# Kernel optimization log

Measured on AMD Instinct MI355X. Metric: run time of the kernel, lower is better.

Reference implementation:

```python
import jax, jax.numpy as jnp
import numpy as np

B, C, D, H, W = 4, 128, 16, 16, 16
HID = 128
EPS = 1e-5


def setup_inputs() -> dict:
    key = jax.random.key(0)
    ks = jax.random.split(key, 10)
    s = 1.0 / np.sqrt(C)
    return {
        "x": jax.random.normal(ks[0], (B, C, D, H, W), dtype=jnp.float32),
        "Wq": jax.random.normal(ks[1], (HID, C), dtype=jnp.float32) * s,
        "bq": jax.random.normal(ks[2], (HID,), dtype=jnp.float32) * s,
        "Wk": jax.random.normal(ks[3], (HID, C), dtype=jnp.float32) * s,
        "bk": jax.random.normal(ks[4], (HID,), dtype=jnp.float32) * s,
        "Wv": jax.random.normal(ks[5], (HID, C), dtype=jnp.float32) * s,
        "bv": jax.random.normal(ks[6], (HID,), dtype=jnp.float32) * s,
        "bn_weight": jax.random.normal(ks[7], (HID,), dtype=jnp.float32),
        "bn_bias": jax.random.normal(ks[8], (HID,), dtype=jnp.float32),
        "gamma": jax.random.normal(ks[9], (1,), dtype=jnp.float32),
    }


def reference(x, Wq, bq, Wk, bk, Wv, bv, bn_weight, bn_bias, gamma):
    b, c, d, h, w = x.shape
    n = d * h * w
    xf = x.reshape(b, c, n)  # [B, C, N]
    # 1x1 conv3d == per-voxel linear: [B, hid, N]
    q = jnp.einsum("hc,bcn->bnh", Wq, xf) + bq  # [B, N, hid] (query permuted)
    k = jnp.einsum("hc,bcn->bhn", Wk, xf) + bk[None, :, None]  # [B, hid, N]
    v = jnp.einsum("hc,bcn->bhn", Wv, xf) + bv[None, :, None]  # [B, hid, N]
    # unscaled attention scores [B, N, N], softmax over last dim
    attn = jax.nn.softmax(jnp.einsum("bih,bhj->bij", q, k), axis=-1)
    # out[b,h,i] = sum_j v[b,h,j] * attn[b,i,j]
    out = jnp.einsum("bhj,bij->bhi", v, attn)  # [B, hid, N]
    # BatchNorm3d (training mode): per-channel stats over (B, N), biased var
    mean = jnp.mean(out, axis=(0, 2), keepdims=True)
    var = jnp.mean(jnp.square(out - mean), axis=(0, 2), keepdims=True)
    out = (out - mean) * jax.lax.rsqrt(var + EPS)
    out = out * bn_weight[None, :, None] + bn_bias[None, :, None]
    out = gamma[0] * out.reshape(b, c, d, h, w) + x
    return out
```

## Files before the change

kernel.cpp:

```cpp
#include <hip/hip_runtime.h>


#define NV 4096
#define LOG2E 1.44269504088896340736f
#define EPSV 1e-5f

typedef float f32x4 __attribute__((ext_vector_type(4)));
typedef short bf16x8 __attribute__((ext_vector_type(8)));
typedef unsigned short u16x4 __attribute__((ext_vector_type(4)));

static __device__ __forceinline__ unsigned short f2bf(float f) {
    union { float f; unsigned u; } v; v.f = f;
    unsigned r = v.u + 0x7FFFu + ((v.u >> 16) & 1u);
    return (unsigned short)(r >> 16);
}
static __device__ __forceinline__ float bf2f(unsigned short u) {
    union { unsigned u; float f; } v; v.u = ((unsigned)u) << 16; return v.f;
}

__global__ __launch_bounds__(256) void convw_kernel(
    const float* __restrict__ Wq, const float* __restrict__ Wk,
    const float* __restrict__ Wv, unsigned short* __restrict__ Wbf)
{
    int i = blockIdx.x * 256 + threadIdx.x;
    const float* src = (i < 16384) ? Wq : (i < 32768 ? Wk : Wv);
    Wbf[i] = f2bf(src[i & 16383]);
}

__global__ __launch_bounds__(256) void xt_kernel(
    const float* __restrict__ x, unsigned short* __restrict__ xT)
{
    __shared__ unsigned short st[64 * 132];
    const int b = blockIdx.x >> 6, n0 = (blockIdx.x & 63) << 6;
    const int t = threadIdx.x;
    #pragma unroll
    for (int it = 0; it < 32; ++it) {
        const int e = it * 256 + t;
        const int c = e >> 6, il = e & 63;
        st[il * 132 + c] = f2bf(x[(((b << 7) + c) << 12) + n0 + il]);
    }
    __syncthreads();
    unsigned short* dst = xT + (((b << 12) + n0) << 7);
    #pragma unroll
    for (int it = 0; it < 32; ++it) {
        const int e = it * 256 + t;
        const int il = e >> 7, c = e & 127;
        dst[(il << 7) + c] = st[il * 132 + c];
    }
}

__global__ __launch_bounds__(256) void proj_kernel(
    const unsigned short* __restrict__ xT,
    const unsigned short* __restrict__ Wbf,
    const float* __restrict__ bq, const float* __restrict__ bk,
    const float* __restrict__ bv,
    unsigned short* __restrict__ Qb, unsigned short* __restrict__ Kb,
    unsigned short* __restrict__ Vb)
{
    __shared__ unsigned short vtile[128 * 66];
    const int bid = blockIdx.x;
    const int m = bid >> 8, b = (bid >> 6) & 3, n0 = (bid & 63) << 6;
    const int t = threadIdx.x, w = t >> 6, lane = t & 63;
    const int quad = lane >> 4, l16 = lane & 15;
    const int vb = n0 + (w << 4);

    bf16x8 af[4];
    {
        const unsigned short* xr = xT + (((b << 12) + vb + l16) << 7) + (quad << 3);
        #pragma unroll
        for (int ck = 0; ck < 4; ++ck) af[ck] = *(const bf16x8*)(xr + (ck << 5));
    }
    const unsigned short* Wm = Wbf + (m << 14);
    const float* bias = (m == 0) ? bq : ((m == 1) ? bk : bv);
    unsigned short* dst = (m == 0) ? Qb : Kb;

    #pragma unroll
    for (int s = 0; s < 8; ++s) {
        const int h = (s << 4) + l16;
        f32x4 acc = {0.f, 0.f, 0.f, 0.f};
        #pragma unroll
        for (int ck = 0; ck < 4; ++ck) {
            bf16x8 wf = *(const bf16x8*)(Wm + (h << 7) + (ck << 5) + (quad << 3));
            acc = __builtin_amdgcn_mfma_f32_16x16x32_bf16(af[ck], wf, acc, 0, 0, 0);
        }
        const float bval = bias[h];
        if (m == 2) {
            #pragma unroll
            for (int r = 0; r < 4; ++r)
                vtile[h * 66 + (w << 4) + (quad << 2) + r] = f2bf(acc[r] + bval);
        } else {
            #pragma unroll
            for (int r = 0; r < 4; ++r) {
                const int n = vb + (quad << 2) + r;
                dst[(((b << 12) + n) << 7) + h] = f2bf(acc[r] + bval);
            }
        }
    }
    if (m == 2) {
        __syncthreads();
        #pragma unroll
        for (int it = 0; it < 32; ++it) {
            const int e = it * 256 + t;
            const int h = e >> 6, il = e & 63;
            Vb[(((b << 7) + h) << 12) + n0 + il] = vtile[h * 66 + il];
        }
    }
}

template<int NSL>
__global__ __launch_bounds__(256, 2) void flash_kernel(
    const unsigned short* __restrict__ Qb,
    const unsigned short* __restrict__ Kb,
    const unsigned short* __restrict__ Vb,
    float* __restrict__ Opart, float* __restrict__ lpart,
    unsigned short* __restrict__ Obuf)
{
    __shared__ unsigned short Kt[64 * 128];
    __shared__ unsigned short Vt[128 * 64];
    __shared__ unsigned short pA[4][32 * 72];
    const int bid = blockIdx.x;
    const int sl = bid >> 7, b = (bid >> 5) & 3, ic = bid & 31;
    const int t = threadIdx.x, w = t >> 6, lane = t & 63;
    const int quad = lane >> 4, l16 = lane & 15;
    const int iw = (ic << 7) + (w << 5);
    const int jbase = sl * (NV / NSL);
    unsigned short* pAw = pA[w];

    const int ktg = t & 15, ktj = t >> 4;
    const int vtg = t & 7,  vth = t >> 3;
    const int kswz = (ktg ^ ktj) << 3;
    const int vswz = (vtg ^ (vth & 7)) << 3;

    bf16x8 qf[2][4];
    #pragma unroll
    for (int half = 0; half < 2; ++half) {
        const unsigned short* qp =
            Qb + (((b << 12) + iw + (half << 4) + l16) << 7) + (quad << 3);
        #pragma unroll
        for (int ck = 0; ck < 4; ++ck) qf[half][ck] = *(const bf16x8*)(qp + (ck << 5));
    }
    f32x4 Oacc[2][8];
    #pragma unroll
    for (int half = 0; half < 2; ++half)
        #pragma unroll
        for (int s = 0; s < 8; ++s) Oacc[half][s] = (f32x4){0.f, 0.f, 0.f, 0.f};
    float lsum0 = 0.f, lsum1 = 0.f;

    const unsigned short* Kbb = Kb + ((long)b << 19);
    const unsigned short* Vbb = Vb + ((long)b << 19);

    for (int t8 = 0; t8 < (NV / NSL) >> 6; ++t8) {
        const int j0 = jbase + (t8 << 6);

        __syncthreads();
        bf16x8 sk[4], sv[4];
        #pragma unroll
        for (int r = 0; r < 4; ++r)
            sk[r] = *(const bf16x8*)(Kbb + ((j0 + (r << 4) + ktj) << 7) + (ktg << 3));
        #pragma unroll
        for (int r = 0; r < 4; ++r)
            sv[r] = *(const bf16x8*)(Vbb + (((r << 5) + vth) << 12) + j0 + (vtg << 3));
        #pragma unroll
        for (int r = 0; r < 4; ++r)
            *(bf16x8*)(Kt + (((r << 4) + ktj) << 7) + kswz) = sk[r];
        #pragma unroll
        for (int r = 0; r < 4; ++r)
            *(bf16x8*)(Vt + (((r << 5) + vth) << 6) + vswz) = sv[r];
        __syncthreads();

        #pragma unroll
        for (int js = 0; js < 4; ++js) {
            bf16x8 kf[4];
            const int krow = ((js << 4) + l16) << 7;
            #pragma unroll
            for (int ck = 0; ck < 4; ++ck)
                kf[ck] = *(const bf16x8*)(Kt + krow + ((((ck << 2) + quad) ^ l16) << 3));
            f32x4 a0 = {0.f, 0.f, 0.f, 0.f}, a1 = {0.f, 0.f, 0.f, 0.f};
            #pragma unroll
            for (int ck = 0; ck < 4; ++ck) {
                a0 = __builtin_amdgcn_mfma_f32_16x16x32_bf16(kf[ck], qf[0][ck], a0, 0, 0, 0);
                a1 = __builtin_amdgcn_mfma_f32_16x16x32_bf16(kf[ck], qf[1][ck], a1, 0, 0, 0);
            }
            u16x4 pk0, pk1;
            float ls0 = 0.f, ls1 = 0.f;
            #pragma unroll
            for (int r = 0; r < 4; ++r) {
                const unsigned short u0 = f2bf(exp2f(a0[r] * LOG2E));
                const unsigned short u1 = f2bf(exp2f(a1[r] * LOG2E));
                pk0[r] = u0; ls0 += bf2f(u0);
                pk1[r] = u1; ls1 += bf2f(u1);
            }
            lsum0 += ls0; lsum1 += ls1;
            const int jc = (js << 4) + (quad << 2);
            *(u16x4*)(pAw + l16 * 72 + jc)        = pk0;
            *(u16x4*)(pAw + (16 + l16) * 72 + jc) = pk1;
        }
        bf16x8 pf[2][2];
        #pragma unroll
        for (int half = 0; half < 2; ++half)
            #pragma unroll
            for (int kh = 0; kh < 2; ++kh)
                pf[half][kh] = *(const bf16x8*)(pAw + ((half << 4) + l16) * 72 +
                                                (kh << 5) + (quad << 3));
        #pragma unroll
        for (int s = 0; s < 8; ++s) {
            const int vrow = ((s << 4) + l16) << 6;
            const bf16x8 v0 = *(const bf16x8*)(Vt + vrow + ((quad ^ (l16 & 7)) << 3));
            const bf16x8 v1 = *(const bf16x8*)(Vt + vrow + (((4 + quad) ^ (l16 & 7)) << 3));
            Oacc[0][s] = __builtin_amdgcn_mfma_f32_16x16x32_bf16(v0, pf[0][0], Oacc[0][s], 0, 0, 0);
            Oacc[0][s] = __builtin_amdgcn_mfma_f32_16x16x32_bf16(v1, pf[0][1], Oacc[0][s], 0, 0, 0);
            Oacc[1][s] = __builtin_amdgcn_mfma_f32_16x16x32_bf16(v0, pf[1][0], Oacc[1][s], 0, 0, 0);
            Oacc[1][s] = __builtin_amdgcn_mfma_f32_16x16x32_bf16(v1, pf[1][1], Oacc[1][s], 0, 0, 0);
        }
    }

    float l0 = lsum0; l0 += __shfl_xor(l0, 16); l0 += __shfl_xor(l0, 32);
    float l1 = lsum1; l1 += __shfl_xor(l1, 16); l1 += __shfl_xor(l1, 32);

    if (NSL == 1) {
        const float rl0 = 1.f / l0, rl1 = 1.f / l1;
        #pragma unroll
        for (int s = 0; s < 8; ++s)
            #pragma unroll
            for (int r = 0; r < 4; ++r) {
                const int h = (s << 4) + (quad << 2) + r;
                Obuf[(((b << 7) + h) << 12) + iw + l16]      = f2bf(Oacc[0][s][r] * rl0);
                Obuf[(((b << 7) + h) << 12) + iw + 16 + l16] = f2bf(Oacc[1][s][r] * rl1);
            }
    } else {
        const int slb = (sl << 2) + b;
        if (quad == 0) {
            lpart[(slb << 12) + iw + l16]      = l0;
            lpart[(slb << 12) + iw + 16 + l16] = l1;
        }
        float* Ob = Opart + ((long)slb << 19);
        #pragma unroll
        for (int half = 0; half < 2; ++half)
            #pragma unroll
            for (int s = 0; s < 8; ++s)
                #pragma unroll
                for (int r = 0; r < 4; ++r) {
                    const int h = (s << 4) + (quad << 2) + r;
                    Ob[(h << 12) + iw + (half << 4) + l16] = Oacc[half][s][r];
                }
    }
}

template<int NSL>
__global__ __launch_bounds__(256) void merge_kernel(
    const float* __restrict__ Opart, const float* __restrict__ lpart,
    unsigned short* __restrict__ Obuf, float* __restrict__ psums)
{
    const int bid = blockIdx.x;
    const int b = bid >> 9, h = (bid >> 2) & 127, iq = bid & 3;
    const int t = threadIdx.x;
    const int ibase = (iq << 10) + (t << 2);
    float a0 = 0.f, a1 = 0.f, a2 = 0.f, a3 = 0.f;
    float t0 = 0.f, t1 = 0.f, t2 = 0.f, t3 = 0.f;
    #pragma unroll
    for (int sl = 0; sl < NSL; ++sl) {
        const int slb = (sl << 2) + b;
        const float4 u  = *(const float4*)(Opart + ((long)slb << 19) + ((long)h << 12) + ibase);
        const float4 lv = *(const float4*)(lpart + (slb << 12) + ibase);
        a0 += u.x; a1 += u.y; a2 += u.z; a3 += u.w;
        t0 += lv.x; t1 += lv.y; t2 += lv.z; t3 += lv.w;
    }
    const float o0 = a0 / t0, o1 = a1 / t1, o2 = a2 / t2, o3 = a3 / t3;
    u16x4 o;
    o[0] = f2bf(o0); o[1] = f2bf(o1); o[2] = f2bf(o2); o[3] = f2bf(o3);
    *(u16x4*)(Obuf + (((b << 7) + h) << 12) + ibase) = o;

    float so  = o0 + o1 + o2 + o3;
    float so2 = o0*o0 + o1*o1 + o2*o2 + o3*o3;
    #pragma unroll
    for (int off = 32; off; off >>= 1) {
        so  += __shfl_down(so, off);
        so2 += __shfl_down(so2, off);
    }
    __shared__ float rb[8];
    const int wv = t >> 6;
    if ((t & 63) == 0) { rb[wv] = so; rb[4 + wv] = so2; }
    __syncthreads();
    if (t == 0) {
        psums[bid]        = rb[0] + rb[1] + rb[2] + rb[3];
        psums[2048 + bid] = rb[4] + rb[5] + rb[6] + rb[7];
    }
}

__global__ __launch_bounds__(256) void bnsum_kernel(
    const unsigned short* __restrict__ Obuf, float* __restrict__ psums)
{
    const int bid = blockIdx.x;
    const int b = bid >> 9, h = (bid >> 2) & 127, iq = bid & 3;
    const int t = threadIdx.x;
    const int ibase = (iq << 10) + (t << 2);
    const u16x4 u = *(const u16x4*)(Obuf + (((b << 7) + h) << 12) + ibase);
    const float x0 = bf2f(u[0]), x1 = bf2f(u[1]), x2 = bf2f(u[2]), x3 = bf2f(u[3]);
    float so  = x0 + x1 + x2 + x3;
    float so2 = x0*x0 + x1*x1 + x2*x2 + x3*x3;
    #pragma unroll
    for (int off = 32; off; off >>= 1) {
        so  += __shfl_down(so, off);
        so2 += __shfl_down(so2, off);
    }
    __shared__ float rb[8];
    const int wv = t >> 6;
    if ((t & 63) == 0) { rb[wv] = so; rb[4 + wv] = so2; }
    __syncthreads();
    if (t == 0) {
        psums[bid]        = rb[0] + rb[1] + rb[2] + rb[3];
        psums[2048 + bid] = rb[4] + rb[5] + rb[6] + rb[7];
    }
}

__global__ __launch_bounds__(256) void final_kernel(
    const unsigned short* __restrict__ Obuf, const float* __restrict__ x,
    const float* __restrict__ psums, const float* __restrict__ bnw,
    const float* __restrict__ bnb, const float* __restrict__ gammap,
    float* __restrict__ out)
{
    const int bid = blockIdx.x;
    const int c = (bid >> 2) & 127;
    const int t = threadIdx.x;
    const int li = t & 15;
    const int pid = ((li >> 2) << 9) + (c << 2) + (li & 3);
    float s  = psums[pid];
    float ss = psums[2048 + pid];
    s += __shfl_xor(s, 1, 16); ss += __shfl_xor(ss, 1, 16);
    s += __shfl_xor(s, 2, 16); ss += __shfl_xor(ss, 2, 16);
    s += __shfl_xor(s, 4, 16); ss += __shfl_xor(ss, 4, 16);
    s += __shfl_xor(s, 8, 16); ss += __shfl_xor(ss, 8, 16);
    const float inv = 1.f / 16384.f;
    const float mean = s * inv;
    const float var  = ss * inv - mean * mean;
    const float g = gammap[0];
    const float scale = bnw[c] * rsqrtf(var + EPSV);
    const float a  = g * scale;
    const float bb = g * (bnb[c] - mean * scale);

    const int base = (bid * 256 + t) << 2;
    const u16x4 u = *(const u16x4*)(Obuf + base);
    const float4 xv = *(const float4*)(x + base);
    float4 r;
    r.x = bf2f(u[0]) * a + bb + xv.x;
    r.y = bf2f(u[1]) * a + bb + xv.y;
    r.z = bf2f(u[2]) * a + bb + xv.z;
    r.w = bf2f(u[3]) * a + bb + xv.w;
    *(float4*)(out + base) = r;
}

extern "C" void kernel_launch(void* const* d_in, const int* in_sizes, int n_in,
                              void* d_out, int out_size, void* d_ws, size_t ws_size,
                              hipStream_t stream) {
    const float* x   = (const float*)d_in[0];
    const float* Wq  = (const float*)d_in[1];
    const float* bq  = (const float*)d_in[2];
    const float* Wk  = (const float*)d_in[3];
    const float* bk  = (const float*)d_in[4];
    const float* Wv  = (const float*)d_in[5];
    const float* bv  = (const float*)d_in[6];
    const float* bnw = (const float*)d_in[7];
    const float* bnb = (const float*)d_in[8];
    const float* gam = (const float*)d_in[9];
    float* out = (float*)d_out;

    char* ws = (char*)d_ws;
    unsigned short* xT   = (unsigned short*)(ws);
    unsigned short* Obuf = (unsigned short*)(ws);
    unsigned short* Qb   = (unsigned short*)(ws + (4u  << 20));
    unsigned short* Kb   = (unsigned short*)(ws + (8u  << 20));
    unsigned short* Vb   = (unsigned short*)(ws + (12u << 20));
    unsigned short* Wbf  = (unsigned short*)(ws + (16u << 20));
    float*          lpart = (float*)(ws + (16u << 20) + (128u << 10));
    float*          psums = (float*)(ws + (16u << 20) + (512u << 10));
    float*          Opart = (float*)(ws + (17u << 20));

    int nsl = 1;
    if      (ws_size >= (17ull << 20) + (32ull << 20)) nsl = 4;
    else if (ws_size >= (17ull << 20) + (16ull << 20)) nsl = 2;

    convw_kernel<<<192, 256, 0, stream>>>(Wq, Wk, Wv, Wbf);
    xt_kernel<<<256, 256, 0, stream>>>(x, xT);
    proj_kernel<<<768, 256, 0, stream>>>(xT, Wbf, bq, bk, bv, Qb, Kb, Vb);
    if (nsl == 4) {
        flash_kernel<4><<<512, 256, 0, stream>>>(Qb, Kb, Vb, Opart, lpart, Obuf);
        merge_kernel<4><<<2048, 256, 0, stream>>>(Opart, lpart, Obuf, psums);
    } else if (nsl == 2) {
        flash_kernel<2><<<256, 256, 0, stream>>>(Qb, Kb, Vb, Opart, lpart, Obuf);
        merge_kernel<2><<<2048, 256, 0, stream>>>(Opart, lpart, Obuf, psums);
    } else {
        flash_kernel<1><<<128, 256, 0, stream>>>(Qb, Kb, Vb, Opart, lpart, Obuf);
        bnsum_kernel<<<2048, 256, 0, stream>>>(Obuf, psums);
    }
    final_kernel<<<2048, 256, 0, stream>>>(Obuf, x, psums, bnw, bnb, gam, out);
}
```

Measured before the change: 159.5 us.

## Store split-KV partials in bf16, raise split count, pack P via perm

Partial attention outputs are now written as bf16 instead of fp32, halving the Opart traffic. That freed workspace lets the host pick 8 KV slices (1024 blocks) instead of 4 when space allows, so more CUs have work. The softmax numerators are now packed to bf16 with a byte-permute that truncates rather than rounds, and the row sum is taken from the unrounded fp32 exponentials. This trades some accuracy (bf16 partials, truncation, a mismatch between the sum and the stored P) for more parallelism and less merge bandwidth.

```diff
diff --git a/kernel.cpp b/kernel.cpp
--- a/kernel.cpp
+++ b/kernel.cpp
@@ -8,6 +8,7 @@
 typedef float f32x4 __attribute__((ext_vector_type(4)));
 typedef short bf16x8 __attribute__((ext_vector_type(8)));
 typedef unsigned short u16x4 __attribute__((ext_vector_type(4)));
+typedef unsigned int u32x2 __attribute__((ext_vector_type(2)));
 
 static __device__ __forceinline__ unsigned short f2bf(float f) {
     union { float f; unsigned u; } v; v.f = f;
@@ -16,6 +17,9 @@
 }
 static __device__ __forceinline__ float bf2f(unsigned short u) {
     union { unsigned u; float f; } v; v.u = ((unsigned)u) << 16; return v.f;
+}
+static __device__ __forceinline__ unsigned fbits(float f) {
+    union { float f; unsigned u; } v; v.f = f; return v.u;
 }
 
 __global__ __launch_bounds__(256) void convw_kernel(
@@ -112,7 +116,7 @@
     const unsigned short* __restrict__ Qb,
     const unsigned short* __restrict__ Kb,
     const unsigned short* __restrict__ Vb,
-    float* __restrict__ Opart, float* __restrict__ lpart,
+    unsigned short* __restrict__ Opart, float* __restrict__ lpart,
     unsigned short* __restrict__ Obuf)
 {
     __shared__ unsigned short Kt[64 * 128];
@@ -181,19 +185,22 @@
                 a0 = __builtin_amdgcn_mfma_f32_16x16x32_bf16(kf[ck], qf[0][ck], a0, 0, 0, 0);
                 a1 = __builtin_amdgcn_mfma_f32_16x16x32_bf16(kf[ck], qf[1][ck], a1, 0, 0, 0);
             }
-            u16x4 pk0, pk1;
-            float ls0 = 0.f, ls1 = 0.f;
+            f32x4 e0, e1;
             #pragma unroll
             for (int r = 0; r < 4; ++r) {
-                const unsigned short u0 = f2bf(exp2f(a0[r] * LOG2E));
-                const unsigned short u1 = f2bf(exp2f(a1[r] * LOG2E));
-                pk0[r] = u0; ls0 += bf2f(u0);
-                pk1[r] = u1; ls1 += bf2f(u1);
+                e0[r] = exp2f(a0[r] * LOG2E);
+                e1[r] = exp2f(a1[r] * LOG2E);
             }
-            lsum0 += ls0; lsum1 += ls1;
+            lsum0 += (e0[0] + e0[1]) + (e0[2] + e0[3]);
+            lsum1 += (e1[0] + e1[1]) + (e1[2] + e1[3]);
+            u32x2 pk0, pk1;
+            pk0[0] = __builtin_amdgcn_perm(fbits(e0[1]), fbits(e0[0]), 0x07060302u);
+            pk0[1] = __builtin_amdgcn_perm(fbits(e0[3]), fbits(e0[2]), 0x07060302u);
+            pk1[0] = __builtin_amdgcn_perm(fbits(e1[1]), fbits(e1[0]), 0x07060302u);
+            pk1[1] = __builtin_amdgcn_perm(fbits(e1[3]), fbits(e1[2]), 0x07060302u);
             const int jc = (js << 4) + (quad << 2);
-            *(u16x4*)(pAw + l16 * 72 + jc)        = pk0;
-            *(u16x4*)(pAw + (16 + l16) * 72 + jc) = pk1;
+            *(u32x2*)(pAw + l16 * 72 + jc)        = pk0;
+            *(u32x2*)(pAw + (16 + l16) * 72 + jc) = pk1;
         }
         bf16x8 pf[2][2];
         #pragma unroll
@@ -233,7 +240,7 @@
             lpart[(slb << 12) + iw + l16]      = l0;
             lpart[(slb << 12) + iw + 16 + l16] = l1;
         }
-        float* Ob = Opart + ((long)slb << 19);
+        unsigned short* Ob = Opart + ((long)slb << 19);
         #pragma unroll
         for (int half = 0; half < 2; ++half)
             #pragma unroll
@@ -241,14 +248,14 @@
                 #pragma unroll
                 for (int r = 0; r < 4; ++r) {
                     const int h = (s << 4) + (quad << 2) + r;
-                    Ob[(h << 12) + iw + (half << 4) + l16] = Oacc[half][s][r];
+                    Ob[(h << 12) + iw + (half << 4) + l16] = f2bf(Oacc[half][s][r]);
                 }
     }
 }
 
 template<int NSL>
 __global__ __launch_bounds__(256) void merge_kernel(
-    const float* __restrict__ Opart, const float* __restrict__ lpart,
+    const unsigned short* __restrict__ Opart, const float* __restrict__ lpart,
     unsigned short* __restrict__ Obuf, float* __restrict__ psums)
 {
     const int bid = blockIdx.x;
@@ -260,9 +267,9 @@
     #pragma unroll
     for (int sl = 0; sl < NSL; ++sl) {
         const int slb = (sl << 2) + b;
-        const float4 u  = *(const float4*)(Opart + ((long)slb << 19) + ((long)h << 12) + ibase);
+        const u16x4 u  = *(const u16x4*)(Opart + ((long)slb << 19) + ((long)h << 12) + ibase);
         const float4 lv = *(const float4*)(lpart + (slb << 12) + ibase);
-        a0 += u.x; a1 += u.y; a2 += u.z; a3 += u.w;
+        a0 += bf2f(u[0]); a1 += bf2f(u[1]); a2 += bf2f(u[2]); a3 += bf2f(u[3]);
         t0 += lv.x; t1 += lv.y; t2 += lv.z; t3 += lv.w;
     }
     const float o0 = a0 / t0, o1 = a1 / t1, o2 = a2 / t2, o3 = a3 / t3;
@@ -372,17 +379,21 @@
     unsigned short* Vb   = (unsigned short*)(ws + (12u << 20));
     unsigned short* Wbf  = (unsigned short*)(ws + (16u << 20));
     float*          lpart = (float*)(ws + (16u << 20) + (128u << 10));
-    float*          psums = (float*)(ws + (16u << 20) + (512u << 10));
-    float*          Opart = (float*)(ws + (17u << 20));
+    float*          psums = (float*)(ws + (16u << 20) + (640u << 10));
+    unsigned short* Opart = (unsigned short*)(ws + (17u << 20));
 
     int nsl = 1;
-    if      (ws_size >= (17ull << 20) + (32ull << 20)) nsl = 4;
-    else if (ws_size >= (17ull << 20) + (16ull << 20)) nsl = 2;
+    if      (ws_size >= (17ull << 20) + (32ull << 20)) nsl = 8;
+    else if (ws_size >= (17ull << 20) + (16ull << 20)) nsl = 4;
+    else if (ws_size >= (17ull << 20) + (8ull  << 20)) nsl = 2;
 
     convw_kernel<<<192, 256, 0, stream>>>(Wq, Wk, Wv, Wbf);
     xt_kernel<<<256, 256, 0, stream>>>(x, xT);
     proj_kernel<<<768, 256, 0, stream>>>(xT, Wbf, bq, bk, bv, Qb, Kb, Vb);
-    if (nsl == 4) {
+    if (nsl == 8) {
+        flash_kernel<8><<<1024, 256, 0, stream>>>(Qb, Kb, Vb, Opart, lpart, Obuf);
+        merge_kernel<8><<<2048, 256, 0, stream>>>(Opart, lpart, Obuf, psums);
+    } else if (nsl == 4) {
         flash_kernel<4><<<512, 256, 0, stream>>>(Qb, Kb, Vb, Opart, lpart, Obuf);
         merge_kernel<4><<<2048, 256, 0, stream>>>(Opart, lpart, Obuf, psums);
     } else if (nsl == 2) {
```

Result: no change. 160.2 us (+0.5%).
